# Performance work log

Hardware: AMD Instinct MI355X
Metric: run time of the kernel (lower is better)

The kernel has to match this reference:

```python
import jax, jax.numpy as jnp
import numpy as np
import jax.scipy.linalg as jsl

K = 4           # num_hops + 1
N = 4096        # nodes
D = 256         # in_dim == out_dim
S = 32          # subspace_dim
ETA = 0.5
EPS = 0.5


def setup_inputs() -> dict:
    key = jax.random.key(0)
    k1, k2, k3 = jax.random.split(key, 3)
    hops = jax.random.normal(k1, (K, N, D), dtype=jnp.float32)
    A = (jax.random.uniform(k2, (N, N)) < 0.01).astype(jnp.float32)
    A = jnp.maximum(A, A.T)
    A = jnp.fill_diagonal(A, 1.0, inplace=False)
    deg = A.sum(axis=1)
    L = jnp.diag(deg) - A  # graph Laplacian
    # orthonormal subspace bases via QR, as in __init__
    raw = jax.random.normal(k3, (K, D, S), dtype=jnp.float32)
    q, _ = jnp.linalg.qr(raw)
    U = q[:, :, :S]
    hop_weights = jnp.ones((K,), dtype=jnp.float32) / K
    threshold = jnp.full((D,), 0.05, dtype=jnp.float32)
    lambda_lap = jnp.asarray(0.1, dtype=jnp.float32)
    return {"hops": hops, "adj_mask": A, "L": L, "U": U,
            "hop_weights": hop_weights, "threshold": threshold,
            "lambda_lap": lambda_lap}


def reference(hops, adj_mask, L, U, hop_weights, threshold, lambda_lap):
    n = hops.shape[1]
    s = U.shape[-1]
    w = jax.nn.softmax(hop_weights, axis=0)
    mask_add = (1.0 - adj_mask) * -1e9  # [n, n]
    I_s = jnp.eye(s, dtype=hops.dtype)
    agg_total = jnp.zeros((hops.shape[2], n), dtype=hops.dtype)  # [d, n]
    coeff = s / (n * EPS ** 2)
    for k in range(K):  # small fixed hop count
        Uk = U[k]                      # [d, s]
        Zk = Uk.T @ hops[k].T          # [s, n]
        M_k = I_s + coeff * (Zk @ Zk.T)  # [s, s]
        cf = jsl.cho_factor(M_k)
        M_inv = jsl.cho_solve(cf, I_s)   # Cholesky inverse
        MZ = M_inv @ Zk                  # [s, n]
        scores = Zk.T @ MZ + mask_add    # [n, n] Mahalanobis-style attention
        alpha = jax.nn.softmax(scores, axis=1)
        grad_k = Uk @ (MZ @ alpha.T)     # [d, n]
        agg_total = agg_total + w[k] * grad_k
    H_agg = agg_total.T                  # [n, d]
    lap_grad = lambda_lap * (L @ H_agg)
    H_half = hops[0] + ETA * H_agg - ETA * lap_grad
    # soft-threshold (proximal step); in_dim == out_dim so no proj
    H_out = jnp.sign(H_half) * jax.nn.relu(jnp.abs(H_half) - threshold[None, :])
    # orthogonality regularizer over subspace bases
    orth_loss = jnp.asarray(0.0, dtype=hops.dtype)
    for k in range(K):
        UkTUk = U[k].T @ U[k]
        orth_loss = orth_loss + ((UkTUk - I_s) ** 2).sum()
        for l in range(k + 1, K):
            orth_loss = orth_loss + ((U[k].T @ U[l]) ** 2).sum()
    lap_smooth = jnp.sum(H_out * (L @ H_out))  # trace(H^T L H)
    return (H_out, orth_loss, lap_smooth, jax.lax.stop_gradient(w))
```

## Files before the change

### kernel.cpp

```cpp
#include <hip/hip_runtime.h>
#include <cstddef>

typedef unsigned short ushortt;
typedef unsigned int uintt;

static constexpr int Nn = 4096;
static constexpr int Dd = 256;
static constexpr int Ss = 32;
static constexpr int Kk = 4;
static constexpr int ZBLK = 2048;
static constexpr int CAP = 144;
static constexpr int RST = 136;
static constexpr float kEta   = 0.5f;
static constexpr float kCoeff = 0.03125f;

__device__ __forceinline__ float waveReduceSum(float v){
  #pragma unroll
  for (int off = 32; off > 0; off >>= 1) v += __shfl_down(v, off, 64);
  return v;
}
__device__ __forceinline__ float blo(uintt u){ return __uint_as_float(u << 16); }
__device__ __forceinline__ float bhi(uintt u){ return __uint_as_float(u & 0xffff0000u); }
__device__ __forceinline__ ushortt f2b(float x){
  uintt u = __float_as_uint(x);
  uintt r = (u + 0x7fffu + ((u >> 16) & 1u)) >> 16;
  return (ushortt)r;
}
__device__ __forceinline__ float b2f(ushortt u){ return __uint_as_float(((uintt)u) << 16); }

__global__ __launch_bounds__(256) void buildz_kernel(const float* __restrict__ A,
                                                     const float* __restrict__ hw,
                                                     const float* __restrict__ hops,
                                                     const float* __restrict__ U,
                                                     int* __restrict__ deg,
                                                     int* __restrict__ colx,
                                                     float* __restrict__ Zt4,
                                                     float* __restrict__ Ubt,
                                                     float* __restrict__ out){
  int tid = threadIdx.x;
  if (blockIdx.x < ZBLK){
    int b = blockIdx.x;
    int k = b >> 9;
    int i0 = (b & 511) * 8;
    __shared__ float Us[32][132];
    int s = tid & 31, ii = tid >> 5;
    int i = i0 + ii;
    const float4* h4 = (const float4*)(hops + ((size_t)k * Nn + i) * Dd);
    float a0 = 0.f, a1 = 0.f, a2 = 0.f, a3 = 0.f;
    #pragma unroll
    for (int half = 0; half < 2; half++){
      if (half) __syncthreads();
      for (int t = tid; t < 32 * 128; t += 256){
        int d = t >> 5, s2 = t & 31;
        Us[s2][d] = U[(size_t)k * Dd * Ss + (size_t)(half * 128 + d) * Ss + s2];
      }
      __syncthreads();
      const float4* u4 = (const float4*)(&Us[s][0]);
      const float4* hh = h4 + half * 32;
      #pragma unroll 8
      for (int dq = 0; dq < 32; dq++){
        float4 h = hh[dq];
        float4 u = u4[dq];
        a0 = fmaf(h.x, u.x, a0);
        a1 = fmaf(h.y, u.y, a1);
        a2 = fmaf(h.z, u.z, a2);
        a3 = fmaf(h.w, u.w, a3);
      }
    }
    Zt4[(size_t)i * 128 + k * 32 + s] = (a0 + a1) + (a2 + a3);
    if (b < 128){
      int idx = b * 256 + tid;
      int c = idx >> 8, d = idx & 255;
      int kk = c >> 5, s2 = c & 31;
      Ubt[idx] = U[(size_t)kk * Dd * Ss + (size_t)d * Ss + s2];
    }
    return;
  }
  int i = blockIdx.x - ZBLK;
  if (i == 0 && tid == 0){
    out[1048576] = 0.f;
    out[1048577] = 0.f;
    float a0=hw[0], a1=hw[1], a2=hw[2], a3=hw[3];
    float mx = fmaxf(fmaxf(a0,a1), fmaxf(a2,a3));
    float e0=expf(a0-mx), e1=expf(a1-mx), e2=expf(a2-mx), e3=expf(a3-mx);
    float s = e0+e1+e2+e3;
    out[1048578]=e0/s; out[1048579]=e1/s; out[1048580]=e2/s; out[1048581]=e3/s;
  }
  int lane = tid & 63, w = tid >> 6;
  __shared__ int wbuf[4][96];
  __shared__ int wcnt[4];
  const float4* row4 = (const float4*)(A + (size_t)i * Nn);
  int cnt = 0;
  int base = w * 256;
  unsigned long long below = (lane == 63) ? 0x7fffffffffffffffull : ((1ull << lane) - 1ull);
  #pragma unroll
  for (int it = 0; it < 4; it++){
    int c4 = base + it * 64 + lane;
    float4 v = row4[c4];
    bool f0 = (v.x != 0.f), f1 = (v.y != 0.f), f2 = (v.z != 0.f), f3 = (v.w != 0.f);
    unsigned long long m0 = __ballot(f0), m1 = __ballot(f1),
                       m2 = __ballot(f2), m3 = __ballot(f3);
    int pre = __popcll(m0 & below) + __popcll(m1 & below)
            + __popcll(m2 & below) + __popcll(m3 & below);
    int pos = cnt + pre;
    int j0 = c4 * 4;
    if (f0){ if (pos < 96) wbuf[w][pos] = j0;     pos++; }
    if (f1){ if (pos < 96) wbuf[w][pos] = j0 + 1; pos++; }
    if (f2){ if (pos < 96) wbuf[w][pos] = j0 + 2; pos++; }
    if (f3){ if (pos < 96) wbuf[w][pos] = j0 + 3; pos++; }
    cnt += __popcll(m0) + __popcll(m1) + __popcll(m2) + __popcll(m3);
  }
  if (cnt > 96) cnt = 96;
  if (lane == 0) wcnt[w] = cnt;
  __syncthreads();
  int off = 0;
  for (int ww = 0; ww < w; ww++) off += wcnt[ww];
  int total = wcnt[0] + wcnt[1] + wcnt[2] + wcnt[3];
  for (int idx = lane; idx < cnt; idx += 64){
    int p = off + idx;
    if (p < CAP) colx[(size_t)i * CAP + p] = wbuf[w][idx];
  }
  if (tid == 0) deg[i] = (total < CAP) ? total : CAP;
}

__global__ __launch_bounds__(256) void mpart_kernel(const float* __restrict__ Zt4,
                                                    float* __restrict__ Mpart){
  int b = blockIdx.x;
  int k = b >> 4, ch = b & 15;
  int i0 = ch * 256;
  __shared__ float zs[256][33];
  for (int t = threadIdx.x; t < 256 * 32; t += 256){
    int ii = t >> 5, s = t & 31;
    zs[ii][s] = Zt4[(size_t)(i0 + ii) * 128 + k * 32 + s];
  }
  __syncthreads();
  int tid = threadIdx.x;
  int s2 = tid & 31, s1b = tid >> 5;
  float a0=0.f, a1=0.f, a2=0.f, a3=0.f;
  for (int ii = 0; ii < 256; ii++){
    float zc = zs[ii][s2];
    a0 = fmaf(zs[ii][s1b],      zc, a0);
    a1 = fmaf(zs[ii][8 + s1b],  zc, a1);
    a2 = fmaf(zs[ii][16 + s1b], zc, a2);
    a3 = fmaf(zs[ii][24 + s1b], zc, a3);
  }
  float* outp = Mpart + (size_t)b * 1024;
  outp[0 * 256 + tid] = a0;
  outp[1 * 256 + tid] = a1;
  outp[2 * 256 + tid] = a2;
  outp[3 * 256 + tid] = a3;
}

__global__ __launch_bounds__(256) void inv_kernel(const float* __restrict__ Mpart,
                                                  float* __restrict__ Minv){
  __shared__ float Msh[4][32][33];
  int tid = threadIdx.x;
  for (int e = tid; e < 4096; e += 256){
    int k = e >> 10, rc = e & 1023;
    float s = 0.f;
    for (int ch = 0; ch < 16; ch++) s += Mpart[(size_t)(k * 16 + ch) * 1024 + rc];
    int r = rc >> 5, c = rc & 31;
    Msh[k][r][c] = kCoeff * s + ((r == c) ? 1.f : 0.f);
  }
  __syncthreads();
  int k = tid >> 6, lane = tid & 63, r = lane & 31, half = lane >> 5;
  float a[32];
  #pragma unroll
  for (int j = 0; j < 32; j++) a[j] = half ? ((r == j) ? 1.f : 0.f) : Msh[k][r][j];
  #pragma unroll
  for (int p = 0; p < 32; p++){
    float app = __shfl(a[p], p, 64);
    float pinv = 1.f / app;
    float f = __shfl(a[p], r, 64);
    #pragma unroll
    for (int j = 0; j < 32; j++){
      float pr = __shfl(a[j], p + (half << 5), 64) * pinv;
      a[j] = (r == p) ? pr : fmaf(-f, pr, a[j]);
    }
  }
  if (half){
    #pragma unroll
    for (int j = 0; j < 32; j++) Minv[(size_t)k * 1024 + r * 32 + j] = a[j];
  }
}

__global__ __launch_bounds__(256) void mz_kernel(const float* __restrict__ Zt4,
                                                 const float* __restrict__ Minv,
                                                 ushortt* __restrict__ MZb){
  int b = blockIdx.x;
  int k = b >> 7;
  int i0 = (b & 127) * 32;
  __shared__ float mi[32][33];
  __shared__ float zs[32][33];
  for (int t = threadIdx.x; t < 1024; t += 256){
    int ii = t >> 5, s2 = t & 31;
    mi[ii][s2] = Minv[(size_t)k * 1024 + t];
    zs[ii][s2] = Zt4[(size_t)(i0 + ii) * 128 + k * 32 + s2];
  }
  __syncthreads();
  int s = threadIdx.x & 31;
  for (int rr = 0; rr < 4; rr++){
    int ii = rr * 8 + (threadIdx.x >> 5);
    float acc = 0.f;
    #pragma unroll
    for (int s2 = 0; s2 < 32; s2++) acc = fmaf(mi[s][s2], zs[ii][s2], acc);
    MZb[(size_t)(i0 + ii) * 128 + k * 32 + s] = f2b(acc);
  }
}

__global__ __launch_bounds__(256) void agg_kernel(const float* __restrict__ Zt4,
                                                  const ushortt* __restrict__ MZb,
                                                  const float* __restrict__ wvec,
                                                  const int* __restrict__ deg,
                                                  const int* __restrict__ colx,
                                                  float* __restrict__ Vw){
  int i = blockIdx.x, tid = threadIdx.x;
  int lane = tid & 63, k = tid >> 6;
  __shared__ __align__(16) ushortt rows[CAP * RST];
  __shared__ int cols[CAP];
  __shared__ __align__(16) float zi[128];
  __shared__ float sc[4][CAP + 8];
  int m = deg[i];
  if (tid < 128) zi[tid] = Zt4[(size_t)i * 128 + tid];
  if (tid < m)  cols[tid] = colx[(size_t)i * CAP + tid];
  __syncthreads();

  int q = tid & 3, r = tid >> 2;
  float zq[32];
  {
    const float4* z4 = (const float4*)(&zi[q * 32]);
    #pragma unroll
    for (int p = 0; p < 8; p++){
      float4 z = z4[p];
      zq[p*4+0]=z.x; zq[p*4+1]=z.y; zq[p*4+2]=z.z; zq[p*4+3]=z.w;
    }
  }

  for (int t = r; t < m; t += 64){
    int j = cols[t];
    const uint4* src = (const uint4*)(MZb + (size_t)j * 128 + q * 32);
    uint4 q0 = src[0], q1 = src[1], q2 = src[2], q3 = src[3];
    uint4* dst = (uint4*)(rows + (size_t)t * RST + q * 32);
    dst[0] = q0; dst[1] = q1; dst[2] = q2; dst[3] = q3;
    float acc = 0.f;
    acc += blo(q0.x)*zq[0] + bhi(q0.x)*zq[1] + blo(q0.y)*zq[2] + bhi(q0.y)*zq[3];
    acc += blo(q0.z)*zq[4] + bhi(q0.z)*zq[5] + blo(q0.w)*zq[6] + bhi(q0.w)*zq[7];
    acc += blo(q1.x)*zq[8] + bhi(q1.x)*zq[9] + blo(q1.y)*zq[10]+ bhi(q1.y)*zq[11];
    acc += blo(q1.z)*zq[12]+ bhi(q1.z)*zq[13]+ blo(q1.w)*zq[14]+ bhi(q1.w)*zq[15];
    acc += blo(q2.x)*zq[16]+ bhi(q2.x)*zq[17]+ blo(q2.y)*zq[18]+ bhi(q2.y)*zq[19];
    acc += blo(q2.z)*zq[20]+ bhi(q2.z)*zq[21]+ blo(q2.w)*zq[22]+ bhi(q2.w)*zq[23];
    acc += blo(q3.x)*zq[24]+ bhi(q3.x)*zq[25]+ blo(q3.y)*zq[26]+ bhi(q3.y)*zq[27];
    acc += blo(q3.z)*zq[28]+ bhi(q3.z)*zq[29]+ blo(q3.w)*zq[30]+ bhi(q3.w)*zq[31];
    sc[q][t] = acc;
  }
  __syncthreads();

  float lmax = -3.0e38f;
  for (int t = lane; t < m; t += 64) lmax = fmaxf(lmax, sc[k][t]);
  #pragma unroll
  for (int off = 32; off > 0; off >>= 1) lmax = fmaxf(lmax, __shfl_xor(lmax, off, 64));
  float lsum = 0.f;
  for (int t = lane; t < m; t += 64){
    float e = __expf(sc[k][t] - lmax);
    sc[k][t] = e;
    lsum += e;
  }
  #pragma unroll
  for (int off = 32; off > 0; off >>= 1) lsum += __shfl_xor(lsum, off, 64);
  float scale = wvec[k] / lsum;

  int c2 = lane & 15, h = lane >> 4;
  float a0 = 0.f, a1 = 0.f;
  #pragma unroll 4
  for (int t = h; t < m; t += 4){
    uintt u = *(const uintt*)(rows + (size_t)t * RST + k * 32 + c2 * 2);
    float e = sc[k][t];
    a0 = fmaf(blo(u), e, a0);
    a1 = fmaf(bhi(u), e, a1);
  }
  a0 += __shfl_xor(a0, 16, 64); a0 += __shfl_xor(a0, 32, 64);
  a1 += __shfl_xor(a1, 16, 64); a1 += __shfl_xor(a1, 32, 64);
  if (h == 0){
    float2 v2 = make_float2(a0 * scale, a1 * scale);
    *(float2*)(Vw + (size_t)i * 128 + k * 32 + c2 * 2) = v2;
  }
}

__global__ __launch_bounds__(256) void gho_kernel(const float* __restrict__ Vw,
                                                  const float* __restrict__ Ubt,
                                                  const float* __restrict__ hops0,
                                                  const float* __restrict__ thr,
                                                  const float* __restrict__ U,
                                                  const float* __restrict__ lam_ptr,
                                                  const int* __restrict__ deg,
                                                  const int* __restrict__ colx,
                                                  float* __restrict__ out,
                                                  ushortt* __restrict__ Hb){
  int tid = threadIdx.x;
  if (blockIdx.x >= 1024){
    int g = (blockIdx.x - 1024) * 256 + tid;
    int pair = g >> 10;
    int idx = g & 1023;
    int s1 = idx >> 5, s2 = idx & 31;
    const int pk_[10] = {0,0,0,0,1,1,1,2,2,3};
    const int pl_[10] = {0,1,2,3,1,2,3,2,3,3};
    int pk = pk_[pair], pl = pl_[pair];
    const float* Uk = U + (size_t)pk * Dd * Ss;
    const float* Ul = U + (size_t)pl * Dd * Ss;
    float dot = 0.f;
    for (int d = 0; d < Dd; d++) dot += Uk[d * Ss + s1] * Ul[d * Ss + s2];
    float val = dot - ((pk == pl && s1 == s2) ? 1.f : 0.f);
    val *= val;
    val = waveReduceSum(val);
    __shared__ float redo[4];
    if ((tid & 63) == 0) redo[tid >> 6] = val;
    __syncthreads();
    if (tid == 0) atomicAdd(out + 1048576, redo[0] + redo[1] + redo[2] + redo[3]);
    return;
  }
  int i0 = blockIdx.x * 4;
  int lane = tid & 63, w = tid >> 6;
  __shared__ float Cs[4][132];
  __shared__ int cols_s[4][CAP];
  {
    int i = i0 + w;
    int m = deg[i];
    for (int t = lane; t < m; t += 64) cols_s[w][t] = colx[(size_t)i * CAP + t];
    float lam = lam_ptr[0];
    int half = lane >> 5, c32 = lane & 31;
    float4 acc = make_float4(0.f, 0.f, 0.f, 0.f);
    for (int t = half; t < m; t += 2){
      int j = cols_s[w][t];
      float4 v = ((const float4*)(Vw + (size_t)j * 128))[c32];
      acc.x += v.x; acc.y += v.y; acc.z += v.z; acc.w += v.w;
    }
    acc.x += __shfl_xor(acc.x, 32, 64);
    acc.y += __shfl_xor(acc.y, 32, 64);
    acc.z += __shfl_xor(acc.z, 32, 64);
    acc.w += __shfl_xor(acc.w, 32, 64);
    if (half == 0){
      float4 self = ((const float4*)(Vw + (size_t)i * 128))[c32];
      float ca = kEta * (1.f - lam * (float)m);
      float cb = kEta * lam;
      float4 o;
      o.x = fmaf(ca, self.x, cb * acc.x);
      o.y = fmaf(ca, self.y, cb * acc.y);
      o.z = fmaf(ca, self.z, cb * acc.z);
      o.w = fmaf(ca, self.w, cb * acc.w);
      *(float4*)(&Cs[w][c32 * 4]) = o;
    }
  }
  __syncthreads();
  int d4 = tid & 63, g = tid >> 6;
  float4 acc = make_float4(0.f, 0.f, 0.f, 0.f);
  #pragma unroll 4
  for (int c = 0; c < 128; c++){
    float4 ub = ((const float4*)(Ubt + (size_t)c * 256))[d4];
    float cs = Cs[g][c];
    acc.x = fmaf(cs, ub.x, acc.x);
    acc.y = fmaf(cs, ub.y, acc.y);
    acc.z = fmaf(cs, ub.z, acc.z);
    acc.w = fmaf(cs, ub.w, acc.w);
  }
  float4 th = ((const float4*)thr)[d4];
  int i = i0 + g;
  float4 hp = ((const float4*)(hops0 + (size_t)i * 256))[d4];
  float hx = hp.x + acc.x, hy = hp.y + acc.y;
  float hz = hp.z + acc.z, hw = hp.w + acc.w;
  float4 o;
  o.x = copysignf(fmaxf(fabsf(hx) - th.x, 0.f), hx);
  o.y = copysignf(fmaxf(fabsf(hy) - th.y, 0.f), hy);
  o.z = copysignf(fmaxf(fabsf(hz) - th.z, 0.f), hz);
  o.w = copysignf(fmaxf(fabsf(hw) - th.w, 0.f), hw);
  ((float4*)(out + (size_t)i * 256))[d4] = o;
  ushort4 hb;
  hb.x = f2b(o.x); hb.y = f2b(o.y); hb.z = f2b(o.z); hb.w = f2b(o.w);
  *((ushort4*)(Hb + (size_t)i * 256 + d4 * 4)) = hb;
}

__global__ __launch_bounds__(256) void lap_kernel(const float* __restrict__ Hout,
                                                  const ushortt* __restrict__ Hb,
                                                  const int* __restrict__ deg,
                                                  const int* __restrict__ colx,
                                                  float* __restrict__ lap_part){
  int b = blockIdx.x;
  int i = b >> 1, half = b & 1;
  int tid = threadIdx.x;
  int dl = tid & 127, g = tid >> 7;
  int d = half * 128 + dl;
  __shared__ int cols[CAP];
  int m = deg[i];
  if (tid < m) cols[tid] = colx[(size_t)i * CAP + tid];
  __syncthreads();
  float nb = 0.f;
  #pragma unroll 8
  for (int t = g; t < m; t += 2)
    nb += b2f(Hb[(size_t)cols[t] * 256 + d]);
  float hi = Hout[(size_t)i * 256 + d];
  float part = -hi * nb;
  if (g == 0) part = fmaf((float)m * hi, hi, part);
  part = waveReduceSum(part);
  __shared__ float red[4];
  if ((tid & 63) == 0) red[tid >> 6] = part;
  __syncthreads();
  if (tid == 0) lap_part[b] = red[0] + red[1] + red[2] + red[3];
}

__global__ __launch_bounds__(256) void lapred_kernel(const float* __restrict__ lap_part,
                                                     float* __restrict__ out){
  int tid = threadIdx.x;
  float s = 0.f;
  const float4* p4 = (const float4*)lap_part;
  #pragma unroll
  for (int q = 0; q < 8; q++){
    float4 v = p4[q * 256 + tid];
    s += v.x + v.y + v.z + v.w;
  }
  s = waveReduceSum(s);
  __shared__ float red[4];
  if ((tid & 63) == 0) red[tid >> 6] = s;
  __syncthreads();
  if (tid == 0) out[1048577] = red[0] + red[1] + red[2] + red[3];
}

extern "C" void kernel_launch(void* const* d_in, const int* in_sizes, int n_in,
                              void* d_out, int out_size, void* d_ws, size_t ws_size,
                              hipStream_t stream)
{
  const float* hops = (const float*)d_in[0];
  const float* A    = (const float*)d_in[1];
  const float* L    = (const float*)d_in[2];
  const float* U    = (const float*)d_in[3];
  const float* hw   = (const float*)d_in[4];
  const float* thr  = (const float*)d_in[5];
  const float* lam  = (const float*)d_in[6];
  (void)L; (void)in_sizes; (void)n_in; (void)out_size; (void)ws_size;

  float* out = (float*)d_out;
  float* ws  = (float*)d_ws;

  float*   Zt4   = ws;
  float*   Vw    = ws + 524288;
  ushortt* MZb   = (ushortt*)(ws + 1572864);
  ushortt* Hb    = (ushortt*)(ws + 1835008);
  float*   Ubt   = ws + 2359296;
  float*   Mpart = ws + 2392064;
  float*   Minv  = ws + 2457600;
  int*     deg   = (int*)(ws + 2461696);
  int*     colx  = (int*)(ws + 2465792);
  float*   lapp  = ws + 3121152;

  float* w_out = out + 1048578;

  buildz_kernel<<<Nn + ZBLK, 256, 0, stream>>>(A, hw, hops, U, deg, colx, Zt4, Ubt, out);
  mpart_kernel <<<Kk*16, 256, 0, stream>>>(Zt4, Mpart);
  inv_kernel   <<<1, 256, 0, stream>>>(Mpart, Minv);
  mz_kernel    <<<Kk*128, 256, 0, stream>>>(Zt4, Minv, MZb);
  agg_kernel   <<<Nn, 256, 0, stream>>>(Zt4, MZb, w_out, deg, colx, Vw);
  gho_kernel   <<<1064, 256, 0, stream>>>(Vw, Ubt, hops, thr, U, lam, deg, colx, out, Hb);
  lap_kernel   <<<2*Nn, 256, 0, stream>>>(out, Hb, deg, colx, lapp);
  lapred_kernel<<<1, 256, 0, stream>>>(lapp, out);
}
```

Before: 298.8 us.

## Fuse matrix inversion into MZ kernel and vectorize U staging loads

Removes the single-block inversion kernel. Each MZ block now reduces the partial Gram matrices itself, runs the Gauss-Jordan inversion in one wavefront and uses the result directly from shared memory. This drops one launch and one serialized one-block step, in exchange for every one of the 512 blocks repeating the reduction and inversion. It also switches the U tile staging in the Z-building kernel to float4 global loads, and moves Mpart to a different workspace offset.

```diff
diff --git a/kernel.cpp b/kernel.cpp
--- a/kernel.cpp
+++ b/kernel.cpp
@@ -50,9 +50,14 @@
     #pragma unroll
     for (int half = 0; half < 2; half++){
       if (half) __syncthreads();
-      for (int t = tid; t < 32 * 128; t += 256){
-        int d = t >> 5, s2 = t & 31;
-        Us[s2][d] = U[(size_t)k * Dd * Ss + (size_t)(half * 128 + d) * Ss + s2];
+      #pragma unroll
+      for (int g = tid; g < 1024; g += 256){
+        int d = g >> 3, s4 = (g & 7) * 4;
+        float4 u = *(const float4*)(U + ((size_t)k * Dd + half * 128 + d) * Ss + s4);
+        Us[s4 + 0][d] = u.x;
+        Us[s4 + 1][d] = u.y;
+        Us[s4 + 2][d] = u.z;
+        Us[s4 + 3][d] = u.w;
       }
       __syncthreads();
       const float4* u4 = (const float4*)(&Us[s][0]);
@@ -151,56 +156,50 @@
   outp[3 * 256 + tid] = a3;
 }
 
-__global__ __launch_bounds__(256) void inv_kernel(const float* __restrict__ Mpart,
-                                                  float* __restrict__ Minv){
-  __shared__ float Msh[4][32][33];
-  int tid = threadIdx.x;
-  for (int e = tid; e < 4096; e += 256){
-    int k = e >> 10, rc = e & 1023;
-    float s = 0.f;
-    for (int ch = 0; ch < 16; ch++) s += Mpart[(size_t)(k * 16 + ch) * 1024 + rc];
-    int r = rc >> 5, c = rc & 31;
-    Msh[k][r][c] = kCoeff * s + ((r == c) ? 1.f : 0.f);
-  }
-  __syncthreads();
-  int k = tid >> 6, lane = tid & 63, r = lane & 31, half = lane >> 5;
-  float a[32];
-  #pragma unroll
-  for (int j = 0; j < 32; j++) a[j] = half ? ((r == j) ? 1.f : 0.f) : Msh[k][r][j];
-  #pragma unroll
-  for (int p = 0; p < 32; p++){
-    float app = __shfl(a[p], p, 64);
-    float pinv = 1.f / app;
-    float f = __shfl(a[p], r, 64);
-    #pragma unroll
-    for (int j = 0; j < 32; j++){
-      float pr = __shfl(a[j], p + (half << 5), 64) * pinv;
-      a[j] = (r == p) ? pr : fmaf(-f, pr, a[j]);
-    }
-  }
-  if (half){
-    #pragma unroll
-    for (int j = 0; j < 32; j++) Minv[(size_t)k * 1024 + r * 32 + j] = a[j];
-  }
-}
-
-__global__ __launch_bounds__(256) void mz_kernel(const float* __restrict__ Zt4,
-                                                 const float* __restrict__ Minv,
-                                                 ushortt* __restrict__ MZb){
+__global__ __launch_bounds__(256) void mzinv_kernel(const float* __restrict__ Zt4,
+                                                    const float* __restrict__ Mpart,
+                                                    ushortt* __restrict__ MZb){
   int b = blockIdx.x;
   int k = b >> 7;
   int i0 = (b & 127) * 32;
   __shared__ float mi[32][33];
   __shared__ float zs[32][33];
-  for (int t = threadIdx.x; t < 1024; t += 256){
+  int tid = threadIdx.x;
+  for (int t = tid; t < 1024; t += 256){
     int ii = t >> 5, s2 = t & 31;
-    mi[ii][s2] = Minv[(size_t)k * 1024 + t];
     zs[ii][s2] = Zt4[(size_t)(i0 + ii) * 128 + k * 32 + s2];
-  }
-  __syncthreads();
-  int s = threadIdx.x & 31;
+    float s = 0.f;
+    #pragma unroll
+    for (int ch = 0; ch < 16; ch++)
+      s += Mpart[(size_t)(k * 16 + ch) * 1024 + t];
+    mi[ii][s2] = kCoeff * s + ((ii == s2) ? 1.f : 0.f);
+  }
+  __syncthreads();
+  if (tid < 64){
+    int lane = tid, r = lane & 31, half = lane >> 5;
+    float a[32];
+    #pragma unroll
+    for (int j = 0; j < 32; j++) a[j] = half ? ((r == j) ? 1.f : 0.f) : mi[r][j];
+    #pragma unroll
+    for (int p = 0; p < 32; p++){
+      float app = __shfl(a[p], p, 64);
+      float pinv = 1.f / app;
+      float f = __shfl(a[p], r, 64);
+      #pragma unroll
+      for (int j = 0; j < 32; j++){
+        float pr = __shfl(a[j], p + (half << 5), 64) * pinv;
+        a[j] = (r == p) ? pr : fmaf(-f, pr, a[j]);
+      }
+    }
+    if (half){
+      #pragma unroll
+      for (int j = 0; j < 32; j++) mi[r][j] = a[j];
+    }
+  }
+  __syncthreads();
+  int s = tid & 31;
   for (int rr = 0; rr < 4; rr++){
-    int ii = rr * 8 + (threadIdx.x >> 5);
+    int ii = rr * 8 + (tid >> 5);
     float acc = 0.f;
     #pragma unroll
     for (int s2 = 0; s2 < 32; s2++) acc = fmaf(mi[s][s2], zs[ii][s2], acc);
@@ -441,11 +440,10 @@
 
   float*   Zt4   = ws;
   float*   Vw    = ws + 524288;
+  float*   Mpart = ws + 1048576;
   ushortt* MZb   = (ushortt*)(ws + 1572864);
   ushortt* Hb    = (ushortt*)(ws + 1835008);
   float*   Ubt   = ws + 2359296;
-  float*   Mpart = ws + 2392064;
-  float*   Minv  = ws + 2457600;
   int*     deg   = (int*)(ws + 2461696);
   int*     colx  = (int*)(ws + 2465792);
   float*   lapp  = ws + 3121152;
@@ -454,8 +452,7 @@
 
   buildz_kernel<<<Nn + ZBLK, 256, 0, stream>>>(A, hw, hops, U, deg, colx, Zt4, Ubt, out);
   mpart_kernel <<<Kk*16, 256, 0, stream>>>(Zt4, Mpart);
-  inv_kernel   <<<1, 256, 0, stream>>>(Mpart, Minv);
-  mz_kernel    <<<Kk*128, 256, 0, stream>>>(Zt4, Minv, MZb);
+  mzinv_kernel <<<Kk*128, 256, 0, stream>>>(Zt4, Mpart, MZb);
   agg_kernel   <<<Nn, 256, 0, stream>>>(Zt4, MZb, w_out, deg, colx, Vw);
   gho_kernel   <<<1064, 256, 0, stream>>>(Vw, Ubt, hops, thr, U, lam, deg, colx, out, Hb);
   lap_kernel   <<<2*Nn, 256, 0, stream>>>(out, Hb, deg, colx, lapp);
```

After: 288.2 us. -3.6%, faster.
